# Performance work log

Measured on AMD Instinct MI355X. Metric: run time of the kernel, lower is better.

Reference implementation:

```python
import jax, jax.numpy as jnp
import numpy as np

N_NODES = 50000
N_EDGES = 800000
IN_C, HID_C, OUT_C = 128, 128, 64


def setup_inputs() -> dict:
    key = jax.random.key(0)
    k1, k2, k3, k4 = jax.random.split(key, 4)
    x = jax.random.normal(k1, (N_NODES, IN_C), dtype=jnp.float32)
    edge_index = jax.random.randint(k2, (2, N_EDGES), 0, N_NODES, dtype=jnp.int64)
    # Glorot-ish init for weights, zero bias (PyG GCNConv default has bias)
    W1 = jax.random.normal(k3, (IN_C, HID_C), dtype=jnp.float32) * (1.0 / np.sqrt(IN_C))
    b1 = jnp.zeros((HID_C,), dtype=jnp.float32)
    W2 = jax.random.normal(k4, (HID_C, OUT_C), dtype=jnp.float32) * (1.0 / np.sqrt(HID_C))
    b2 = jnp.zeros((OUT_C,), dtype=jnp.float32)
    return {"x": x, "edge_index": edge_index, "W1": W1, "b1": b1, "W2": W2, "b2": b2}


def _gcn_norm(edge_index, num_nodes):
    """PyG gcn_norm: add self-loops, symmetric deg^{-1/2} normalization."""
    loop = jnp.arange(num_nodes, dtype=edge_index.dtype)
    src = jnp.concatenate([edge_index[0], loop])  # [E + N]
    dst = jnp.concatenate([edge_index[1], loop])
    ones = jnp.ones(src.shape[0], dtype=jnp.float32)
    deg = jax.ops.segment_sum(ones, dst, num_segments=num_nodes)  # in-degree incl. self-loop
    dinv = jnp.where(deg > 0, jax.lax.rsqrt(deg), 0.0)
    norm = dinv[src] * dinv[dst]  # [E + N]
    return src, dst, norm


def _gcn_conv(x, W, b, src, dst, norm, num_nodes):
    h = x @ W                                   # [N, C_out] transform first (PyG order)
    msg = h[src] * norm[:, None]                # gather + normalize, [E+N, C_out]
    out = jax.ops.segment_sum(msg, dst, num_segments=num_nodes)  # scatter-add
    return out + b


def reference(x, edge_index, W1, b1, W2, b2):
    N = x.shape[0]
    src, dst, norm = _gcn_norm(edge_index, N)  # graph normalization shared by both layers
    h = jax.nn.relu(_gcn_conv(x, W1, b1, src, dst, norm, N))
    out = _gcn_conv(h, W2, b2, src, dst, norm, N)
    return out
```

## Files before the change

kernel.cpp:

```cpp
#include <hip/hip_runtime.h>
#include <hip/hip_bf16.h>

#define IN_C  128
#define HID_C 128
#define OUT_CC 64
#define BK    128
#define CAPLG 12

using short8  = __attribute__((ext_vector_type(8))) short;
using float4v = __attribute__((ext_vector_type(4))) float;

__device__ __forceinline__ unsigned short f2b(float f) {
    unsigned int u = __float_as_uint(f);
    return (unsigned short)((u + 0x7fffu + ((u >> 16) & 1u)) >> 16);
}
__device__ __forceinline__ unsigned int pack2(float a, float b) {
    return (unsigned int)f2b(a) | ((unsigned int)f2b(b) << 16);
}
__device__ __forceinline__ float2 bf2_to_f2(unsigned int v) {
    float2 r;
    r.x = __uint_as_float(v << 16);
    r.y = __uint_as_float(v & 0xffff0000u);
    return r;
}


__global__ __launch_bounds__(256) void k_setup(const float* __restrict__ W1,
                                               const float* __restrict__ W2,
                                               const int* __restrict__ ei,
                                               unsigned short* __restrict__ w1f,
                                               unsigned short* __restrict__ w2f,
                                               int* __restrict__ flag,
                                               int* __restrict__ bfill, int NBK) {
    int e = blockIdx.x * 256 + threadIdx.x;
    if (e < 16384) {
        int j = e & 7, lane = (e >> 3) & 63, ks = (e >> 9) & 3, nt = e >> 11;
        int k = ks * 32 + ((lane >> 4) << 3) + j;
        int n = nt * 16 + (lane & 15);
        w1f[e] = f2b(W1[k * 128 + n]);
    } else if (e < 16384 + 8192) {
        int e2 = e - 16384;
        int j = e2 & 7, lane = (e2 >> 3) & 63, ks = (e2 >> 9) & 3, nt = e2 >> 11;
        int k = ks * 32 + ((lane >> 4) << 3) + j;
        int n = nt * 16 + (lane & 15);
        w2f[e2] = f2b(W2[k * 64 + n]);
    }
    if (blockIdx.x == 0) {
        for (int i = threadIdx.x; i < NBK; i += 256) bfill[i] = 0;
        if (threadIdx.x == 0) {
            int odd_zero = 1, any_even = 0;
            for (int i = 0; i < 64; ++i) {
                if (ei[2 * i + 1] != 0) odd_zero = 0;
                if (ei[2 * i] != 0) any_even = 1;
            }
            *flag = (odd_zero && any_even) ? 2 : 1;
        }
    }
}

__global__ __launch_bounds__(256) void k_bpart(const int* __restrict__ ei,
                                               const int* __restrict__ flag,
                                               int* __restrict__ bfill,
                                               int* __restrict__ ebuf, int E, int NBK) {
    __shared__ int lh[512];
    __shared__ int lbase[512];
    const int t = threadIdx.x;
    for (int i = t; i < NBK; i += 256) lh[i] = 0;
    __syncthreads();
    const int st = *flag;
    const int base = blockIdx.x * 2048;
    int s[8], d[8];
    #pragma unroll
    for (int j = 0; j < 8; ++j) {
        int i = base + j * 256 + t;
        if (i < E) {
            s[j] = ei[(size_t)st * i];
            d[j] = ei[(size_t)st * ((size_t)E + i)];
            atomicAdd(&lh[d[j] >> 7], 1);
        } else d[j] = -1;
    }
    __syncthreads();
    for (int i = t; i < NBK; i += 256) {
        int c = lh[i];
        lbase[i] = c ? atomicAdd(&bfill[i], c) : 0;
        lh[i] = 0;
    }
    __syncthreads();
    #pragma unroll
    for (int j = 0; j < 8; ++j) {
        if (d[j] >= 0) {
            int b = d[j] >> 7;
            int r = lbase[b] + atomicAdd(&lh[b], 1);
            if (r < (1 << CAPLG))
                ebuf[(b << CAPLG) + r] = s[j] | ((d[j] & (BK - 1)) << 20);
        }
    }
}

__global__ __launch_bounds__(256) void k_blmg1(const int* __restrict__ ebuf,
                                               const int* __restrict__ bfill,
                                               int2* __restrict__ begend,
                                               float* __restrict__ dinv,
                                               int* __restrict__ col,
                                               const float* __restrict__ x,
                                               const unsigned short* __restrict__ w1f,
                                               unsigned short* __restrict__ h,
                                               int N, int NBK) {
    __shared__ unsigned short lds[64 * 136];
    __shared__ int cnt64[64];
    const int t = threadIdx.x;

    if ((int)blockIdx.x < NBK) {
        int* cnt = (int*)lds;
        int* sc  = cnt + BK;
        int* off = sc + BK;
        const int n0 = blockIdx.x * BK;
        const int beg = (int)blockIdx.x << CAPLG;
        const int ecnt = min(bfill[blockIdx.x], 1 << CAPLG);
        if (t < BK) cnt[t] = 0;
        __syncthreads();
        for (int i = t; i < ecnt; i += 256)
            atomicAdd(&cnt[ebuf[beg + i] >> 20], 1);
        __syncthreads();
        if (t < BK) sc[t] = cnt[t];
        __syncthreads();
        for (int o = 1; o < BK; o <<= 1) {
            int v = (t < BK && t >= o) ? sc[t - o] : 0;
            __syncthreads();
            if (t < BK) sc[t] += v;
            __syncthreads();
        }
        if (t < BK) {
            int c = cnt[t];
            off[t] = sc[t] - c;
            if (n0 + t < N) {
                begend[n0 + t] = make_int2(beg + off[t], beg + sc[t]);
                dinv[n0 + t] = rsqrtf((float)c + 1.0f);
            }
            cnt[t] = 0;
        }
        __syncthreads();
        for (int i = t; i < ecnt; i += 256) {
            int e = ebuf[beg + i];
            int dl = e >> 20;
            int p = beg + off[dl] + atomicAdd(&cnt[dl], 1);
            col[p] = e & 0xFFFFF;
        }
        return;
    }

    const int tile = (int)blockIdx.x - NBK;
    const int row0 = tile * 64;
    const int bkt  = row0 >> 7;
    const int half = (row0 >> 6) & 1;
    if (t < 64) cnt64[t] = 0;
    __syncthreads();
    {
        const int ebeg = bkt << CAPLG;
        const int ecnt = min(bfill[bkt], 1 << CAPLG);
        for (int i = t; i < ecnt; i += 256) {
            int dl = ebuf[ebeg + i] >> 20;
            if ((dl >> 6) == half) atomicAdd(&cnt64[dl & 63], 1);
        }
    }
    {
        int r = t >> 2, cc = (t & 3) * 32;
        int grow = row0 + r;
        unsigned int* dst = (unsigned int*)&lds[r * 136 + cc];
        if (grow < N) {
            const float4* src = (const float4*)(x + (size_t)grow * 128 + cc);
            #pragma unroll
            for (int i = 0; i < 8; ++i) {
                float4 v = src[i];
                dst[2 * i]     = pack2(v.x, v.y);
                dst[2 * i + 1] = pack2(v.z, v.w);
            }
        } else {
            #pragma unroll
            for (int i = 0; i < 16; ++i) dst[i] = 0;
        }
    }
    __syncthreads();
    const int w = t >> 6, lane = t & 63;
    const int quad = lane >> 4, m = lane & 15;
    short8 a[4];
    #pragma unroll
    for (int ks = 0; ks < 4; ++ks)
        a[ks] = *(const short8*)&lds[(w * 16 + m) * 136 + ks * 32 + quad * 8];
    float4v acc[8];
    #pragma unroll
    for (int nt = 0; nt < 8; ++nt) acc[nt] = (float4v){0.f, 0.f, 0.f, 0.f};
    const short8* wf = (const short8*)w1f;
    #pragma unroll
    for (int nt = 0; nt < 8; ++nt)
        #pragma unroll
        for (int ks = 0; ks < 4; ++ks)
            acc[nt] = __builtin_amdgcn_mfma_f32_16x16x32_bf16(a[ks], wf[(nt * 4 + ks) * 64 + lane],
                                                              acc[nt], 0, 0, 0);
    float drr[4];
    #pragma unroll
    for (int r = 0; r < 4; ++r) {
        int lr = w * 16 + quad * 4 + r;
        drr[r] = rsqrtf((float)cnt64[lr] + 1.0f);
    }
    #pragma unroll
    for (int nt = 0; nt < 8; ++nt)
        #pragma unroll
        for (int r = 0; r < 4; ++r) {
            int grow = row0 + w * 16 + quad * 4 + r;
            if (grow < N) h[(size_t)grow * 128 + nt * 16 + m] = f2b(acc[nt][r] * drr[r]);
        }
}

__global__ __launch_bounds__(256) void k_aggmg2(const uint4* __restrict__ feat,
                                                const int2* __restrict__ begend,
                                                const int* __restrict__ col,
                                                const float* __restrict__ dinv,
                                                const float* __restrict__ b1,
                                                const unsigned short* __restrict__ w2f,
                                                unsigned short* __restrict__ h2, int N) {
    __shared__ unsigned short lds[16 * 136];
    __shared__ float dvs[16];
    const int grp = threadIdx.x >> 4;
    const int l16 = threadIdx.x & 15;
    const int node = blockIdx.x * 16 + grp;
    float a0 = 0.f, a1 = 0.f, a2 = 0.f, a3 = 0.f, a4 = 0.f, a5 = 0.f, a6 = 0.f, a7 = 0.f;
    if (node < N) {
        const float dd = dinv[node];
        if (l16 == 0) dvs[grp] = dd;
        const int2 be = begend[node];
        const int beg = be.x, end = be.y;
        {
            uint4 sv = feat[(size_t)node * 16 + l16];
            float2 q;
            q = bf2_to_f2(sv.x); a0 = q.x; a1 = q.y;
            q = bf2_to_f2(sv.y); a2 = q.x; a3 = q.y;
            q = bf2_to_f2(sv.z); a4 = q.x; a5 = q.y;
            q = bf2_to_f2(sv.w); a6 = q.x; a7 = q.y;
        }
        int e = beg;
        for (; e + 4 <= end; e += 4) {
            int s0 = col[e], s1 = col[e + 1], s2 = col[e + 2], s3 = col[e + 3];
            uint4 u0 = feat[(size_t)s0 * 16 + l16];
            uint4 u1 = feat[(size_t)s1 * 16 + l16];
            uint4 u2 = feat[(size_t)s2 * 16 + l16];
            uint4 u3 = feat[(size_t)s3 * 16 + l16];
            float2 q;
            q = bf2_to_f2(u0.x); a0 += q.x; a1 += q.y;
            q = bf2_to_f2(u0.y); a2 += q.x; a3 += q.y;
            q = bf2_to_f2(u0.z); a4 += q.x; a5 += q.y;
            q = bf2_to_f2(u0.w); a6 += q.x; a7 += q.y;
            q = bf2_to_f2(u1.x); a0 += q.x; a1 += q.y;
            q = bf2_to_f2(u1.y); a2 += q.x; a3 += q.y;
            q = bf2_to_f2(u1.z); a4 += q.x; a5 += q.y;
            q = bf2_to_f2(u1.w); a6 += q.x; a7 += q.y;
            q = bf2_to_f2(u2.x); a0 += q.x; a1 += q.y;
            q = bf2_to_f2(u2.y); a2 += q.x; a3 += q.y;
            q = bf2_to_f2(u2.z); a4 += q.x; a5 += q.y;
            q = bf2_to_f2(u2.w); a6 += q.x; a7 += q.y;
            q = bf2_to_f2(u3.x); a0 += q.x; a1 += q.y;
            q = bf2_to_f2(u3.y); a2 += q.x; a3 += q.y;
            q = bf2_to_f2(u3.z); a4 += q.x; a5 += q.y;
            q = bf2_to_f2(u3.w); a6 += q.x; a7 += q.y;
        }
        for (; e < end; ++e) {
            int s = col[e];
            uint4 u = feat[(size_t)s * 16 + l16];
            float2 q;
            q = bf2_to_f2(u.x); a0 += q.x; a1 += q.y;
            q = bf2_to_f2(u.y); a2 += q.x; a3 += q.y;
            q = bf2_to_f2(u.z); a4 += q.x; a5 += q.y;
            q = bf2_to_f2(u.w); a6 += q.x; a7 += q.y;
        }
        float4 ba = ((const float4*)b1)[2 * l16];
        float4 bb = ((const float4*)b1)[2 * l16 + 1];
        a0 = fmaxf(a0 * dd + ba.x, 0.0f);
        a1 = fmaxf(a1 * dd + ba.y, 0.0f);
        a2 = fmaxf(a2 * dd + ba.z, 0.0f);
        a3 = fmaxf(a3 * dd + ba.w, 0.0f);
        a4 = fmaxf(a4 * dd + bb.x, 0.0f);
        a5 = fmaxf(a5 * dd + bb.y, 0.0f);
        a6 = fmaxf(a6 * dd + bb.z, 0.0f);
        a7 = fmaxf(a7 * dd + bb.w, 0.0f);
    } else if (l16 == 0) dvs[grp] = 0.f;
    {
        uint4 o;
        o.x = pack2(a0, a1);
        o.y = pack2(a2, a3);
        o.z = pack2(a4, a5);
        o.w = pack2(a6, a7);
        *(uint4*)&lds[grp * 136 + l16 * 8] = o;
    }
    __syncthreads();
    const int w = threadIdx.x >> 6, lane = threadIdx.x & 63;
    const int quad = lane >> 4, m = lane & 15;
    short8 a[4];
    #pragma unroll
    for (int ks = 0; ks < 4; ++ks)
        a[ks] = *(const short8*)&lds[m * 136 + ks * 32 + quad * 8];
    float4v acc = (float4v){0.f, 0.f, 0.f, 0.f};
    const short8* wf = (const short8*)w2f;
    #pragma unroll
    for (int ks = 0; ks < 4; ++ks)
        acc = __builtin_amdgcn_mfma_f32_16x16x32_bf16(a[ks], wf[(w * 4 + ks) * 64 + lane],
                                                      acc, 0, 0, 0);
    const int node0 = blockIdx.x * 16;
    #pragma unroll
    for (int r = 0; r < 4; ++r) {
        int gn = node0 + quad * 4 + r;
        if (gn < N) h2[(size_t)gn * 64 + w * 16 + m] = f2b(acc[r] * dvs[quad * 4 + r]);
    }
}

__global__ __launch_bounds__(256) void k_agg64(const uint2* __restrict__ feat,
                                               const int2* __restrict__ begend,
                                               const int* __restrict__ col,
                                               const float* __restrict__ dinv,
                                               const float* __restrict__ bias,
                                               float* __restrict__ out, int N) {
    const int grp = threadIdx.x >> 4;
    const int l16 = threadIdx.x & 15;
    const int node = blockIdx.x * 16 + grp;
    if (node >= N) return;
    const float dd = dinv[node];
    const int2 be = begend[node];
    const int beg = be.x, end = be.y;
    float a0, a1, a2, a3;
    {
        uint2 sv = feat[(size_t)node * 16 + l16];
        float2 q;
        q = bf2_to_f2(sv.x); a0 = q.x; a1 = q.y;
        q = bf2_to_f2(sv.y); a2 = q.x; a3 = q.y;
    }
    int e = beg;
    for (; e + 4 <= end; e += 4) {
        int s0 = col[e], s1 = col[e + 1], s2 = col[e + 2], s3 = col[e + 3];
        uint2 u0 = feat[(size_t)s0 * 16 + l16];
        uint2 u1 = feat[(size_t)s1 * 16 + l16];
        uint2 u2 = feat[(size_t)s2 * 16 + l16];
        uint2 u3 = feat[(size_t)s3 * 16 + l16];
        float2 q;
        q = bf2_to_f2(u0.x); a0 += q.x; a1 += q.y;
        q = bf2_to_f2(u0.y); a2 += q.x; a3 += q.y;
        q = bf2_to_f2(u1.x); a0 += q.x; a1 += q.y;
        q = bf2_to_f2(u1.y); a2 += q.x; a3 += q.y;
        q = bf2_to_f2(u2.x); a0 += q.x; a1 += q.y;
        q = bf2_to_f2(u2.y); a2 += q.x; a3 += q.y;
        q = bf2_to_f2(u3.x); a0 += q.x; a1 += q.y;
        q = bf2_to_f2(u3.y); a2 += q.x; a3 += q.y;
    }
    for (; e < end; ++e) {
        int s = col[e];
        uint2 u = feat[(size_t)s * 16 + l16];
        float2 q;
        q = bf2_to_f2(u.x); a0 += q.x; a1 += q.y;
        q = bf2_to_f2(u.y); a2 += q.x; a3 += q.y;
    }
    float4 b = ((const float4*)bias)[l16];
    float4 o;
    o.x = a0 * dd + b.x;
    o.y = a1 * dd + b.y;
    o.z = a2 * dd + b.z;
    o.w = a3 * dd + b.w;
    ((float4*)out)[(size_t)node * 16 + l16] = o;
}

extern "C" void kernel_launch(void* const* d_in, const int* in_sizes, int n_in,
                              void* d_out, int out_size, void* d_ws, size_t ws_size,
                              hipStream_t stream) {
    const float* x  = (const float*)d_in[0];
    const int*   ei = (const int*)d_in[1];
    const float* W1 = (const float*)d_in[2];
    const float* b1 = (const float*)d_in[3];
    const float* W2 = (const float*)d_in[4];
    const float* b2 = (const float*)d_in[5];

    const int N = in_sizes[0] / IN_C;
    const int E = in_sizes[1] / 2;
    const int NBK  = (N + BK - 1) / BK;
    const int NCHK = (E + 2047) / 2048;
    const int NT1  = (N + 63) / 64;

    char* ws = (char*)d_ws;
    int*            flag    = (int*)(ws + 0);
    int*            bfill   = (int*)(ws + 64);
    int2*           begend  = (int2*)(ws + 4096);
    float*          dinv    = (float*)(ws + 404480);
    unsigned short* w1f     = (unsigned short*)(ws + 604672);
    unsigned short* w2f     = (unsigned short*)(ws + 637440);
    int*            ebuf    = (int*)(ws + 655360);
    int*            col     = (int*)(ws + 7061504);
    unsigned short* h       = (unsigned short*)(ws + 13467904);
    unsigned short* h2      = (unsigned short*)(ws + 26267904);

    k_setup<<<96, 256, 0, stream>>>(W1, W2, ei, w1f, w2f, flag, bfill, NBK);

    k_bpart<<<NCHK, 256, 0, stream>>>(ei, flag, bfill, ebuf, E, NBK);

    k_blmg1<<<NBK + NT1, 256, 0, stream>>>(ebuf, bfill, begend, dinv, col,
                                           x, w1f, h, N, NBK);

    k_aggmg2<<<(N + 15) / 16, 256, 0, stream>>>((const uint4*)h, begend, col, dinv, b1,
                                                w2f, h2, N);

    k_agg64<<<(N + 15) / 16, 256, 0, stream>>>((const uint2*)h2, begend, col, dinv, b2,
                                               (float*)d_out, N);
}
```

Before: 168.0 us.

## Merge setup into partition kernel, prefetch neighbor indices, widen layer-2 gather lanes

Removes the separate setup kernel: the weight bf16 swizzle now runs in extra blocks of the edge-partition kernel, the bucket counters are cleared with hipMemsetAsync, and every partition block detects the int64 layout itself using a wave ballot. Both aggregation kernels now software-prefetch the next four column indices while gathering the current four rows. The 64-channel aggregation uses 8 lanes per node with 16-byte loads instead of 16 lanes with 8-byte loads, so each block handles 32 nodes. Together these cut launch count and dependent-load latency, at the cost of every partition block redundantly re-checking the layout and fewer threads working on each node.

```diff
diff --git a/kernel.cpp b/kernel.cpp
--- a/kernel.cpp
+++ b/kernel.cpp
@@ -25,49 +25,43 @@
 }
 
 
-__global__ __launch_bounds__(256) void k_setup(const float* __restrict__ W1,
+__global__ __launch_bounds__(256) void k_bpart(const int* __restrict__ ei,
+                                               int* __restrict__ bfill,
+                                               int* __restrict__ ebuf, int E, int NBK,
+                                               int NCHK,
+                                               const float* __restrict__ W1,
                                                const float* __restrict__ W2,
-                                               const int* __restrict__ ei,
                                                unsigned short* __restrict__ w1f,
-                                               unsigned short* __restrict__ w2f,
-                                               int* __restrict__ flag,
-                                               int* __restrict__ bfill, int NBK) {
-    int e = blockIdx.x * 256 + threadIdx.x;
-    if (e < 16384) {
-        int j = e & 7, lane = (e >> 3) & 63, ks = (e >> 9) & 3, nt = e >> 11;
-        int k = ks * 32 + ((lane >> 4) << 3) + j;
-        int n = nt * 16 + (lane & 15);
-        w1f[e] = f2b(W1[k * 128 + n]);
-    } else if (e < 16384 + 8192) {
-        int e2 = e - 16384;
-        int j = e2 & 7, lane = (e2 >> 3) & 63, ks = (e2 >> 9) & 3, nt = e2 >> 11;
-        int k = ks * 32 + ((lane >> 4) << 3) + j;
-        int n = nt * 16 + (lane & 15);
-        w2f[e2] = f2b(W2[k * 64 + n]);
-    }
-    if (blockIdx.x == 0) {
-        for (int i = threadIdx.x; i < NBK; i += 256) bfill[i] = 0;
-        if (threadIdx.x == 0) {
-            int odd_zero = 1, any_even = 0;
-            for (int i = 0; i < 64; ++i) {
-                if (ei[2 * i + 1] != 0) odd_zero = 0;
-                if (ei[2 * i] != 0) any_even = 1;
-            }
-            *flag = (odd_zero && any_even) ? 2 : 1;
-        }
-    }
-}
-
-__global__ __launch_bounds__(256) void k_bpart(const int* __restrict__ ei,
-                                               const int* __restrict__ flag,
-                                               int* __restrict__ bfill,
-                                               int* __restrict__ ebuf, int E, int NBK) {
+                                               unsigned short* __restrict__ w2f) {
+    const int t = threadIdx.x;
+    if ((int)blockIdx.x >= NCHK) {
+        int e = ((int)blockIdx.x - NCHK) * 256 + t;
+        if (e < 16384) {
+            int j = e & 7, lane = (e >> 3) & 63, ks = (e >> 9) & 3, nt = e >> 11;
+            int k = ks * 32 + ((lane >> 4) << 3) + j;
+            int n = nt * 16 + (lane & 15);
+            w1f[e] = f2b(W1[k * 128 + n]);
+        } else if (e < 16384 + 8192) {
+            int e2 = e - 16384;
+            int j = e2 & 7, lane = (e2 >> 3) & 63, ks = (e2 >> 9) & 3, nt = e2 >> 11;
+            int k = ks * 32 + ((lane >> 4) << 3) + j;
+            int n = nt * 16 + (lane & 15);
+            w2f[e2] = f2b(W2[k * 64 + n]);
+        }
+        return;
+    }
     __shared__ int lh[512];
     __shared__ int lbase[512];
-    const int t = threadIdx.x;
+    __shared__ int s_st;
     for (int i = t; i < NBK; i += 256) lh[i] = 0;
-    __syncthreads();
-    const int st = *flag;
+    if (t < 64) {
+        int ev = ei[2 * t], od = ei[2 * t + 1];
+        unsigned long long onz = __ballot(od != 0);
+        unsigned long long enz = __ballot(ev != 0);
+        if (t == 0) s_st = (onz == 0ull && enz != 0ull) ? 2 : 1;
+    }
+    __syncthreads();
+    const int st = s_st;
     const int base = blockIdx.x * 2048;
     int s[8], d[8];
     #pragma unroll
@@ -212,6 +206,12 @@
         }
 }
 
+#define ACC16(u) { float2 q; \
+    q = bf2_to_f2(u.x); a0 += q.x; a1 += q.y; \
+    q = bf2_to_f2(u.y); a2 += q.x; a3 += q.y; \
+    q = bf2_to_f2(u.z); a4 += q.x; a5 += q.y; \
+    q = bf2_to_f2(u.w); a6 += q.x; a7 += q.y; }
+
 __global__ __launch_bounds__(256) void k_aggmg2(const uint4* __restrict__ feat,
                                                 const int2* __restrict__ begend,
                                                 const int* __restrict__ col,
@@ -229,7 +229,7 @@
         const float dd = dinv[node];
         if (l16 == 0) dvs[grp] = dd;
         const int2 be = begend[node];
-        const int beg = be.x, end = be.y;
+        int e = be.x; const int end = be.y;
         {
             uint4 sv = feat[(size_t)node * 16 + l16];
             float2 q;
@@ -238,39 +238,28 @@
             q = bf2_to_f2(sv.z); a4 = q.x; a5 = q.y;
             q = bf2_to_f2(sv.w); a6 = q.x; a7 = q.y;
         }
-        int e = beg;
-        for (; e + 4 <= end; e += 4) {
-            int s0 = col[e], s1 = col[e + 1], s2 = col[e + 2], s3 = col[e + 3];
-            uint4 u0 = feat[(size_t)s0 * 16 + l16];
-            uint4 u1 = feat[(size_t)s1 * 16 + l16];
-            uint4 u2 = feat[(size_t)s2 * 16 + l16];
-            uint4 u3 = feat[(size_t)s3 * 16 + l16];
-            float2 q;
-            q = bf2_to_f2(u0.x); a0 += q.x; a1 += q.y;
-            q = bf2_to_f2(u0.y); a2 += q.x; a3 += q.y;
-            q = bf2_to_f2(u0.z); a4 += q.x; a5 += q.y;
-            q = bf2_to_f2(u0.w); a6 += q.x; a7 += q.y;
-            q = bf2_to_f2(u1.x); a0 += q.x; a1 += q.y;
-            q = bf2_to_f2(u1.y); a2 += q.x; a3 += q.y;
-            q = bf2_to_f2(u1.z); a4 += q.x; a5 += q.y;
-            q = bf2_to_f2(u1.w); a6 += q.x; a7 += q.y;
-            q = bf2_to_f2(u2.x); a0 += q.x; a1 += q.y;
-            q = bf2_to_f2(u2.y); a2 += q.x; a3 += q.y;
-            q = bf2_to_f2(u2.z); a4 += q.x; a5 += q.y;
-            q = bf2_to_f2(u2.w); a6 += q.x; a7 += q.y;
-            q = bf2_to_f2(u3.x); a0 += q.x; a1 += q.y;
-            q = bf2_to_f2(u3.y); a2 += q.x; a3 += q.y;
-            q = bf2_to_f2(u3.z); a4 += q.x; a5 += q.y;
-            q = bf2_to_f2(u3.w); a6 += q.x; a7 += q.y;
+        int c0, c1, c2, c3;
+        if (e + 4 <= end) { c0 = col[e]; c1 = col[e + 1]; c2 = col[e + 2]; c3 = col[e + 3]; }
+        for (; e + 8 <= end; e += 4) {
+            int n0 = col[e + 4], n1 = col[e + 5], n2 = col[e + 6], n3 = col[e + 7];
+            uint4 u0 = feat[(size_t)c0 * 16 + l16];
+            uint4 u1 = feat[(size_t)c1 * 16 + l16];
+            uint4 u2 = feat[(size_t)c2 * 16 + l16];
+            uint4 u3 = feat[(size_t)c3 * 16 + l16];
+            ACC16(u0) ACC16(u1) ACC16(u2) ACC16(u3)
+            c0 = n0; c1 = n1; c2 = n2; c3 = n3;
+        }
+        if (e + 4 <= end) {
+            uint4 u0 = feat[(size_t)c0 * 16 + l16];
+            uint4 u1 = feat[(size_t)c1 * 16 + l16];
+            uint4 u2 = feat[(size_t)c2 * 16 + l16];
+            uint4 u3 = feat[(size_t)c3 * 16 + l16];
+            ACC16(u0) ACC16(u1) ACC16(u2) ACC16(u3)
+            e += 4;
         }
         for (; e < end; ++e) {
-            int s = col[e];
-            uint4 u = feat[(size_t)s * 16 + l16];
-            float2 q;
-            q = bf2_to_f2(u.x); a0 += q.x; a1 += q.y;
-            q = bf2_to_f2(u.y); a2 += q.x; a3 += q.y;
-            q = bf2_to_f2(u.z); a4 += q.x; a5 += q.y;
-            q = bf2_to_f2(u.w); a6 += q.x; a7 += q.y;
+            uint4 u = feat[(size_t)col[e] * 16 + l16];
+            ACC16(u)
         }
         float4 ba = ((const float4*)b1)[2 * l16];
         float4 bb = ((const float4*)b1)[2 * l16 + 1];
@@ -312,57 +301,65 @@
     }
 }
 
-__global__ __launch_bounds__(256) void k_agg64(const uint2* __restrict__ feat,
+__global__ __launch_bounds__(256) void k_agg64(const uint4* __restrict__ feat,
                                                const int2* __restrict__ begend,
                                                const int* __restrict__ col,
                                                const float* __restrict__ dinv,
                                                const float* __restrict__ bias,
                                                float* __restrict__ out, int N) {
-    const int grp = threadIdx.x >> 4;
-    const int l16 = threadIdx.x & 15;
-    const int node = blockIdx.x * 16 + grp;
+    const int grp = threadIdx.x >> 3;
+    const int l8  = threadIdx.x & 7;
+    const int node = blockIdx.x * 32 + grp;
     if (node >= N) return;
     const float dd = dinv[node];
     const int2 be = begend[node];
-    const int beg = be.x, end = be.y;
-    float a0, a1, a2, a3;
+    int e = be.x; const int end = be.y;
+    float a0, a1, a2, a3, a4, a5, a6, a7;
     {
-        uint2 sv = feat[(size_t)node * 16 + l16];
+        uint4 sv = feat[(size_t)node * 8 + l8];
         float2 q;
         q = bf2_to_f2(sv.x); a0 = q.x; a1 = q.y;
         q = bf2_to_f2(sv.y); a2 = q.x; a3 = q.y;
-    }
-    int e = beg;
-    for (; e + 4 <= end; e += 4) {
-        int s0 = col[e], s1 = col[e + 1], s2 = col[e + 2], s3 = col[e + 3];
-        uint2 u0 = feat[(size_t)s0 * 16 + l16];
-        uint2 u1 = feat[(size_t)s1 * 16 + l16];
-        uint2 u2 = feat[(size_t)s2 * 16 + l16];
-        uint2 u3 = feat[(size_t)s3 * 16 + l16];
-        float2 q;
-        q = bf2_to_f2(u0.x); a0 += q.x; a1 += q.y;
-        q = bf2_to_f2(u0.y); a2 += q.x; a3 += q.y;
-        q = bf2_to_f2(u1.x); a0 += q.x; a1 += q.y;
-        q = bf2_to_f2(u1.y); a2 += q.x; a3 += q.y;
-        q = bf2_to_f2(u2.x); a0 += q.x; a1 += q.y;
-        q = bf2_to_f2(u2.y); a2 += q.x; a3 += q.y;
-        q = bf2_to_f2(u3.x); a0 += q.x; a1 += q.y;
-        q = bf2_to_f2(u3.y); a2 += q.x; a3 += q.y;
+        q = bf2_to_f2(sv.z); a4 = q.x; a5 = q.y;
+        q = bf2_to_f2(sv.w); a6 = q.x; a7 = q.y;
+    }
+    int c0, c1, c2, c3;
+    if (e + 4 <= end) { c0 = col[e]; c1 = col[e + 1]; c2 = col[e + 2]; c3 = col[e + 3]; }
+    for (; e + 8 <= end; e += 4) {
+        int n0 = col[e + 4], n1 = col[e + 5], n2 = col[e + 6], n3 = col[e + 7];
+        uint4 u0 = feat[(size_t)c0 * 8 + l8];
+        uint4 u1 = feat[(size_t)c1 * 8 + l8];
+        uint4 u2 = feat[(size_t)c2 * 8 + l8];
+        uint4 u3 = feat[(size_t)c3 * 8 + l8];
+        ACC16(u0) ACC16(u1) ACC16(u2) ACC16(u3)
+        c0 = n0; c1 = n1; c2 = n2; c3 = n3;
+    }
+    if (e + 4 <= end) {
+        uint4 u0 = feat[(size_t)c0 * 8 + l8];
+        uint4 u1 = feat[(size_t)c1 * 8 + l8];
+        uint4 u2 = feat[(size_t)c2 * 8 + l8];
+        uint4 u3 = feat[(size_t)c3 * 8 + l8];
+        ACC16(u0) ACC16(u1) ACC16(u2) ACC16(u3)
+        e += 4;
     }
     for (; e < end; ++e) {
-        int s = col[e];
-        uint2 u = feat[(size_t)s * 16 + l16];
-        float2 q;
-        q = bf2_to_f2(u.x); a0 += q.x; a1 += q.y;
-        q = bf2_to_f2(u.y); a2 += q.x; a3 += q.y;
-    }
-    float4 b = ((const float4*)bias)[l16];
-    float4 o;
-    o.x = a0 * dd + b.x;
-    o.y = a1 * dd + b.y;
-    o.z = a2 * dd + b.z;
-    o.w = a3 * dd + b.w;
-    ((float4*)out)[(size_t)node * 16 + l16] = o;
+        uint4 u = feat[(size_t)col[e] * 8 + l8];
+        ACC16(u)
+    }
+    float4 ba = ((const float4*)bias)[2 * l8];
+    float4 bb = ((const float4*)bias)[2 * l8 + 1];
+    float4 o1, o2;
+    o1.x = a0 * dd + ba.x;
+    o1.y = a1 * dd + ba.y;
+    o1.z = a2 * dd + ba.z;
+    o1.w = a3 * dd + ba.w;
+    o2.x = a4 * dd + bb.x;
+    o2.y = a5 * dd + bb.y;
+    o2.z = a6 * dd + bb.z;
+    o2.w = a7 * dd + bb.w;
+    float4* op = (float4*)out + (size_t)node * 16 + 2 * l8;
+    op[0] = o1;
+    op[1] = o2;
 }
 
 extern "C" void kernel_launch(void* const* d_in, const int* in_sizes, int n_in,
@@ -382,7 +379,6 @@
     const int NT1  = (N + 63) / 64;
 
     char* ws = (char*)d_ws;
-    int*            flag    = (int*)(ws + 0);
     int*            bfill   = (int*)(ws + 64);
     int2*           begend  = (int2*)(ws + 4096);
     float*          dinv    = (float*)(ws + 404480);
@@ -393,9 +389,10 @@
     unsigned short* h       = (unsigned short*)(ws + 13467904);
     unsigned short* h2      = (unsigned short*)(ws + 26267904);
 
-    k_setup<<<96, 256, 0, stream>>>(W1, W2, ei, w1f, w2f, flag, bfill, NBK);
-
-    k_bpart<<<NCHK, 256, 0, stream>>>(ei, flag, bfill, ebuf, E, NBK);
+    hipMemsetAsync(bfill, 0, NBK * sizeof(int), stream);
+
+    k_bpart<<<NCHK + 96, 256, 0, stream>>>(ei, bfill, ebuf, E, NBK, NCHK,
+                                           W1, W2, w1f, w2f);
 
     k_blmg1<<<NBK + NT1, 256, 0, stream>>>(ebuf, bfill, begend, dinv, col,
                                            x, w1f, h, N, NBK);
@@ -403,6 +400,6 @@
     k_aggmg2<<<(N + 15) / 16, 256, 0, stream>>>((const uint4*)h, begend, col, dinv, b1,
                                                 w2f, h2, N);
 
-    k_agg64<<<(N + 15) / 16, 256, 0, stream>>>((const uint2*)h2, begend, col, dinv, b2,
+    k_agg64<<<(N + 31) / 32, 256, 0, stream>>>((const uint4*)h2, begend, col, dinv, b2,
                                                (float*)d_out, N);
 }
```

Result: faster. 160.5 us (-4.5%).
